# Kernel optimization log

Measured on AMD Instinct MI355X. Metric: run time of the kernel, lower is better.

Reference implementation:

```python
import jax, jax.numpy as jnp
import numpy as np

B, S, H, D = 16, 512, 12, 64          # batch, seq, heads, head_dim
HID = H * D                            # 768
MAX_POS = 512
CHAR_HP = 0.5
WORD_HP = 0.5


def setup_inputs() -> dict:
    key = jax.random.key(0)
    ks = jax.random.split(key, 12)
    s = 0.02
    return {
        "hidden_states": jax.random.normal(ks[0], (B, S, HID), jnp.float32),
        "attention_mask": jnp.zeros((B, 1, 1, S), jnp.float32),
        "character_level_matrix": jax.random.randint(ks[1], (B, S, S), 0, 8),
        "word_level_matrix": jax.random.randint(ks[2], (B, S, S), 0, 8),
        "Wq": jax.random.normal(ks[3], (HID, HID), jnp.float32) * s,
        "bq": jnp.zeros((HID,), jnp.float32),
        "Wk": jax.random.normal(ks[4], (HID, HID), jnp.float32) * s,
        "bk": jnp.zeros((HID,), jnp.float32),
        "Wv": jax.random.normal(ks[5], (HID, HID), jnp.float32) * s,
        "bv": jnp.zeros((HID,), jnp.float32),
        "dist_emb": jax.random.normal(ks[6], (2 * MAX_POS - 1, D), jnp.float32) * s,
        "char_emb": jax.random.normal(ks[7], (8, 1), jnp.float32) * s,
        "word_emb": jax.random.normal(ks[8], (8, 1), jnp.float32) * s,
    }


def reference(hidden_states, attention_mask, character_level_matrix,
              word_level_matrix, Wq, bq, Wk, bk, Wv, bv,
              dist_emb, char_emb, word_emb):
    # level nn-embedding lookup: [B,S,S] int -> [B,S,S] float
    char_bias = char_emb[character_level_matrix][..., 0]
    word_bias = word_emb[word_level_matrix][..., 0]

    def heads(x):  # [B,S,HID] -> [B,H,S,D]
        return x.reshape(B, S, H, D).transpose(0, 2, 1, 3)

    q = heads(hidden_states @ Wq.T + bq)
    k = heads(hidden_states @ Wk.T + bk)
    v = heads(hidden_states @ Wv.T + bv)

    scores = jnp.einsum('bhld,bhrd->bhlr', q, k)
    # level biases broadcast over heads
    scores = scores + CHAR_HP * char_bias[:, None] + WORD_HP * word_bias[:, None]

    # relative_key_query positional scores
    pos = jnp.arange(S)
    distance = pos[:, None] - pos[None, :]
    pe = dist_emb[distance + MAX_POS - 1]  # [S(l), S(r), D]
    scores = scores + jnp.einsum('bhld,lrd->bhlr', q, pe) \
                    + jnp.einsum('bhrd,lrd->bhlr', k, pe)

    scores = scores / jnp.sqrt(jnp.float32(D)) + attention_mask
    probs = jax.nn.softmax(scores, axis=-1)
    ctx = jnp.einsum('bhlr,bhrd->bhld', probs, v)
    return ctx.transpose(0, 2, 1, 3).reshape(B, S, HID)
```

## Files before the change

kernel.cpp:

```cpp
#include <hip/hip_runtime.h>
#include <stdint.h>

#define Bv 16
#define Sv 512
#define Hv 12
#define Dv 64
#define HIDv 768

typedef __attribute__((ext_vector_type(8))) short bf8_t;
typedef __attribute__((ext_vector_type(4))) float f32x4;
typedef __attribute__((ext_vector_type(8))) unsigned short u16x8;
typedef __attribute__((ext_vector_type(4))) unsigned short u16x4;

__device__ __forceinline__ float b2f(unsigned short u){
    union { unsigned int i; float f; } x; x.i = ((unsigned int)u) << 16; return x.f;
}
__device__ __forceinline__ unsigned short f2b(float f){
    union { float f; unsigned int i; } x; x.f = f;
    unsigned int r = x.i + 0x7fff + ((x.i >> 16) & 1);
    return (unsigned short)(r >> 16);
}
__device__ __forceinline__ void gload16(const unsigned short* g, unsigned short* l){
    __builtin_amdgcn_global_load_lds(
        (const __attribute__((address_space(1))) void*)g,
        (__attribute__((address_space(3))) void*)l, 16, 0, 0);
}

#define RS 0.18033688f
#define LOG2E 1.44269504f

__global__ void cvt_bf16(const float* __restrict__ src, unsigned short* __restrict__ dst, int n4){
    int i = blockIdx.x * 256 + threadIdx.x;
    int stride = gridDim.x * 256;
    for (; i < n4; i += stride){
        float4 v = ((const float4*)src)[i];
        u16x4 o = { f2b(v.x), f2b(v.y), f2b(v.z), f2b(v.w) };
        ((u16x4*)dst)[i] = o;
    }
}

__global__ void cvt_w3(const float* __restrict__ a, const float* __restrict__ b,
                       const float* __restrict__ c, unsigned short* __restrict__ dst, int n4each){
    int i = blockIdx.x * 256 + threadIdx.x;
    if (i >= 3*n4each) return;
    int which = i / n4each, j = i - which*n4each;
    const float* src = which == 0 ? a : (which == 1 ? b : c);
    float4 v = ((const float4*)src)[j];
    u16x4 o = { f2b(v.x), f2b(v.y), f2b(v.z), f2b(v.w) };
    ((u16x4*)dst)[i] = o;
}

__global__ __launch_bounds__(256) void prep_bias_t(
    const int* __restrict__ cmat, const int* __restrict__ wmat,
    const float* __restrict__ mask, const float* __restrict__ ce, const float* __restrict__ we,
    unsigned short* __restrict__ lvlt)
{
    __shared__ float tab[64];
    __shared__ float mrow[64];
    const int t = threadIdx.x;
    const int blk = blockIdx.x;
    const int c8 = blk & 7, lt = (blk >> 3) & 7, b = blk >> 6;
    if (t < 64) tab[t] = (0.5f*ce[t>>3] + 0.5f*we[t&7]) * RS;
    if (t >= 64 && t < 128) mrow[t-64] = mask[b*512 + c8*64 + (t-64)] * LOG2E;
    __syncthreads();
    const int w = t >> 6, lane = t & 63, g = lane >> 4, cc = lane & 15;
    const int llb = lt*64 + w*16 + g*4;
    const int rlb = c8*64 + cc;
    unsigned short o[16];
    #pragma unroll
    for (int reg = 0; reg < 4; ++reg){
        const int* cr = cmat + ((size_t)b*512 + llb + reg)*512 + rlb;
        const int* wr = wmat + ((size_t)b*512 + llb + reg)*512 + rlb;
        #pragma unroll
        for (int i = 0; i < 4; ++i){
            int cv = cr[i*16], wv = wr[i*16];
            o[reg*4 + i] = f2b(tab[(cv<<3)|wv] + mrow[i*16 + cc]);
        }
    }
    unsigned short* dst = lvlt + ((size_t)blk*256 + t)*16;
    *(u16x8*)dst       = *(u16x8*)&o[0];
    *(u16x8*)(dst + 8) = *(u16x8*)&o[8];
}

__global__ __launch_bounds__(256,3) void qkv_gemm(
    const unsigned short* __restrict__ Xb,
    const unsigned short* __restrict__ Wb,
    const float* __restrict__ bq, const float* __restrict__ bk, const float* __restrict__ bv,
    unsigned short* __restrict__ qkb,
    unsigned short* __restrict__ vtb)
{
    __shared__ unsigned short Ab[128*40];
    __shared__ unsigned short Bb[128*40];
    const int t = threadIdx.x;
    const int w = t >> 6, lane = t & 63, g = lane >> 4, cc = lane & 15;
    const int wm = w >> 1, wn = w & 1;
    const int m0 = blockIdx.x * 128;
    const int n0 = blockIdx.y * 128;

    const f32x4 fz = {0.f,0.f,0.f,0.f};
    f32x4 acc[4][4];
    #pragma unroll
    for (int i = 0; i < 4; ++i)
        #pragma unroll
        for (int j = 0; j < 4; ++j) acc[i][j] = fz;

    u16x8 pa[2], pb[2];
    #pragma unroll
    for (int r = 0; r < 2; ++r){
        int chunk = t + r*256; int row = chunk >> 2; int ch = chunk & 3;
        pa[r] = *(const u16x8*)(Xb + (size_t)(m0+row)*768 + ch*8);
        pb[r] = *(const u16x8*)(Wb + (size_t)(n0+row)*768 + ch*8);
    }
    for (int k0 = 0; k0 < 768; k0 += 32){
        __syncthreads();
        #pragma unroll
        for (int r = 0; r < 2; ++r){
            int chunk = t + r*256; int row = chunk >> 2; int ch = chunk & 3;
            *(u16x8*)&Ab[row*40 + ch*8] = pa[r];
            *(u16x8*)&Bb[row*40 + ch*8] = pb[r];
        }
        __syncthreads();
        if (k0 + 32 < 768){
            #pragma unroll
            for (int r = 0; r < 2; ++r){
                int chunk = t + r*256; int row = chunk >> 2; int ch = chunk & 3;
                pa[r] = *(const u16x8*)(Xb + (size_t)(m0+row)*768 + (k0+32) + ch*8);
                pb[r] = *(const u16x8*)(Wb + (size_t)(n0+row)*768 + (k0+32) + ch*8);
            }
        }
        bf8_t af[4], bfr[4];
        #pragma unroll
        for (int mf = 0; mf < 4; ++mf)
            af[mf] = *(const bf8_t*)&Ab[(wm*64 + mf*16 + cc)*40 + g*8];
        #pragma unroll
        for (int nf = 0; nf < 4; ++nf)
            bfr[nf] = *(const bf8_t*)&Bb[(wn*64 + nf*16 + cc)*40 + g*8];
        #pragma unroll
        for (int mf = 0; mf < 4; ++mf)
            #pragma unroll
            for (int nf = 0; nf < 4; ++nf)
                acc[mf][nf] = __builtin_amdgcn_mfma_f32_16x16x32_bf16(af[mf], bfr[nf], acc[mf][nf], 0,0,0);
    }

    const int b  = m0 >> 9;
    const int s0 = (m0 & 511) + wm*64;
    const int nbase = n0 + wn*64;
    const int proj = nbase / 768;
    const int nin0 = nbase % 768;
    const float* bias = proj == 0 ? bq : (proj == 1 ? bk : bv);
    #pragma unroll
    for (int nf = 0; nf < 4; ++nf){
        int nin = nin0 + nf*16 + cc;
        int h = nin >> 6, d = nin & 63;
        float bvv = bias[nin];
        #pragma unroll
        for (int mf = 0; mf < 4; ++mf){
            int s = s0 + mf*16 + g*4;
            if (proj < 2){
                unsigned short* base = qkb + (((((size_t)proj*Bv + b)*Hv + h)*Sv + s)*Dv + d);
                #pragma unroll
                for (int r2 = 0; r2 < 4; ++r2)
                    base[(size_t)r2*Dv] = f2b(acc[mf][nf][r2] + bvv);
            } else {
                u16x4 o = { f2b(acc[mf][nf][0]+bvv), f2b(acc[mf][nf][1]+bvv),
                            f2b(acc[mf][nf][2]+bvv), f2b(acc[mf][nf][3]+bvv) };
                *(u16x4*)(vtb + ((((size_t)b*Hv + h)*Dv + d)*Sv + s)) = o;
            }
        }
    }
}

__global__ __launch_bounds__(256,2) void attn(
    const unsigned short* __restrict__ qkb,
    const unsigned short* __restrict__ vtb,
    const unsigned short* __restrict__ deb,
    const unsigned short* __restrict__ lvlt,
    float* __restrict__ out)
{
    __shared__ __align__(16) unsigned short sm[37632];
    unsigned short* ks   = sm;
    unsigned short* vsq  = sm + 4096;
    unsigned short* P    = sm + 12288;
    unsigned short* des  = sm + 16384;
    float*          t1c  = (float*)(sm + 24576);
    unsigned short* t2c  = sm + 33280;

    const int t = threadIdx.x, w = t >> 6, lane = t & 63, g = lane >> 4, cc = lane & 15;
    const int lr8 = lane >> 3, lc8 = lane & 7;

    const int wg = blockIdx.x;
    const int xcd = wg & 7, inner = wg >> 3;
    const int b  = ((inner & 1) << 3) | xcd;
    const int r2 = inner >> 1;
    const int h  = r2 % 12, lt = r2 / 12;
    const int l0 = lt * 64;

    const unsigned short* qp = qkb + ((((size_t)0*Bv + b)*Hv + h)*Sv + l0)*Dv;
    const unsigned short* kp = qkb + ((((size_t)1*Bv + b)*Hv + h)*Sv)*Dv;
    const unsigned short* vp = vtb + (((size_t)b*Hv + h)*Dv)*Sv;
    const unsigned short* lvbase = lvlt + (((size_t)b*8 + lt)*8)*256*16 + (size_t)t*16;

    const f32x4 fz = {0.f,0.f,0.f,0.f};
    const int llb = w*16 + g*4;
    const int R   = 3 - w;
    const int rl2b = R*16 + g*4;

    auto stage_k = [&](int r0){
        #pragma unroll
        for (int j = 0; j < 2; ++j){
            int row = w*16 + j*8 + lr8;
            int ch  = lc8 ^ (row & 7);
            gload16(kp + (size_t)(r0 + row)*64 + ch*8, ks + w*1024 + j*512);
        }
    };
    auto stage_de = [&](int r0){
        const int base = l0 - r0 + 448;
        #pragma unroll
        for (int j = 0; j < 4; ++j){
            int row = w*32 + j*8 + lr8;
            int gr = base + row; if (gr > 1022) gr = 1022;
            int ch  = lc8 ^ (row & 7);
            gload16(deb + (size_t)gr*64 + ch*8, des + w*2048 + j*512);
        }
    };
    auto stage_v = [&](int r0, unsigned short* vdst){
        #pragma unroll
        for (int j = 0; j < 2; ++j){
            int row = w*16 + j*8 + lr8;
            int ch  = lc8 ^ (row & 7);
            gload16(vp + (size_t)row*512 + r0 + ch*8, vdst + w*1024 + j*512);
        }
    };

    bf8_t qf0, qf1;
    {
        int qrow = w*16 + cc;
        qf0 = *(const bf8_t*)(qp + (size_t)qrow*64 + g*8);
        qf1 = *(const bf8_t*)(qp + (size_t)qrow*64 + (g+4)*8);
    }
    stage_k(0); stage_de(0); stage_v(0, vsq);
    __syncthreads();

    float l_run[4] = {0.f,0.f,0.f,0.f};
    f32x4 ctx[4] = {fz,fz,fz,fz};

    for (int c8 = 0; c8 < 8; ++c8){
        const int r0 = c8 * 64;
        unsigned short* vcur = vsq + (c8 & 1) * 4096;
        unsigned short* vnxt = vsq + ((c8 + 1) & 1) * 4096;

        u16x8 lva = *(const u16x8*)(lvbase + (size_t)c8*256*16);
        u16x8 lvb = *(const u16x8*)(lvbase + (size_t)c8*256*16 + 8);

        __builtin_amdgcn_s_setprio(1);
        f32x4 accs[4];
        bf8_t kf0, kf1;
        #pragma unroll
        for (int i = 0; i < 4; ++i){
            int row = i*16 + cc;
            bf8_t b0 = *(const bf8_t*)&ks[row*64 + ((g       ^ (row & 7))*8)];
            bf8_t b1 = *(const bf8_t*)&ks[row*64 + (((g + 4) ^ (row & 7))*8)];
            if (i == R){ kf0 = b0; kf1 = b1; }
            f32x4 a = fz;
            a = __builtin_amdgcn_mfma_f32_16x16x32_bf16(qf0, b0, a, 0,0,0);
            a = __builtin_amdgcn_mfma_f32_16x16x32_bf16(qf1, b1, a, 0,0,0);
            accs[i] = a;
        }
        #pragma unroll
        for (int i = 0; i < 5; ++i){
            int jrow = (w + i)*16 + cc;
            bf8_t d0 = *(const bf8_t*)&des[jrow*64 + ((g       ^ (jrow & 7))*8)];
            bf8_t d1 = *(const bf8_t*)&des[jrow*64 + (((g + 4) ^ (jrow & 7))*8)];
            f32x4 a1 = fz, a2 = fz;
            a1 = __builtin_amdgcn_mfma_f32_16x16x32_bf16(qf0, d0, a1, 0,0,0);
            a1 = __builtin_amdgcn_mfma_f32_16x16x32_bf16(qf1, d1, a1, 0,0,0);
            a2 = __builtin_amdgcn_mfma_f32_16x16x32_bf16(kf0, d0, a2, 0,0,0);
            a2 = __builtin_amdgcn_mfma_f32_16x16x32_bf16(kf1, d1, a2, 0,0,0);
            #pragma unroll
            for (int reg = 0; reg < 4; ++reg){
                int rl1 = 4*g + reg - 16*i - cc + 63;
                if (rl1 >= 0 && rl1 < 64) t1c[rl1*68 + llb + reg] = a1[reg];
                int ll2 = 4*g + reg + 16*i + cc - 15;
                if (ll2 >= 0 && ll2 < 64) t2c[(rl2b + reg)*68 + ll2] = f2b(a2[reg]);
            }
        }
        __builtin_amdgcn_s_setprio(0);
        __syncthreads();

        if (c8 < 7){ stage_k(r0 + 64); stage_de(r0 + 64); stage_v(r0 + 64, vnxt); }

        f32x4 t1v4[4];
        u16x4 t2v4[4];
        #pragma unroll
        for (int i = 0; i < 4; ++i){
            t1v4[i] = *(const f32x4*)&t1c[(16*i + cc)*68 + llb];
            t2v4[i] = *(const u16x4*)&t2c[(16*i + cc)*68 + llb];
        }
        #pragma unroll
        for (int reg = 0; reg < 4; ++reg){
            int ll = llb + reg;
            float ps = 0.f;
            #pragma unroll
            for (int i = 0; i < 4; ++i){
                float lvv = b2f(reg < 2 ? (unsigned short)lva[reg*4 + i]
                                        : (unsigned short)lvb[(reg-2)*4 + i]);
                float sv = (accs[i][reg] + t1v4[i][reg] + b2f((unsigned short)t2v4[i][reg])) * RS + lvv;
                float p = __builtin_amdgcn_exp2f(sv);
                ps += p;
                int rl = i*16 + cc;
                P[ll*64 + (((rl >> 3) ^ (ll & 7)) << 3) + (rl & 7)] = f2b(p);
            }
            ps += __shfl_xor(ps, 1); ps += __shfl_xor(ps, 2);
            ps += __shfl_xor(ps, 4); ps += __shfl_xor(ps, 8);
            l_run[reg] += ps;
        }

        __builtin_amdgcn_s_setprio(1);
        #pragma unroll
        for (int kh = 0; kh < 2; ++kh){
            int prow = w*16 + cc;
            bf8_t pf = *(const bf8_t*)&P[prow*64 + (((g + 4*kh) ^ (prow & 7)) << 3)];
            #pragma unroll
            for (int nf = 0; nf < 4; ++nf){
                int vr = nf*16 + cc;
                bf8_t vf = *(const bf8_t*)&vcur[vr*64 + (((g + 4*kh) ^ (vr & 7))*8)];
                ctx[nf] = __builtin_amdgcn_mfma_f32_16x16x32_bf16(pf, vf, ctx[nf], 0,0,0);
            }
        }
        __builtin_amdgcn_s_setprio(0);

        if (c8 < 7)
            __syncthreads();
    }

    #pragma unroll
    for (int nf = 0; nf < 4; ++nf){
        #pragma unroll
        for (int reg = 0; reg < 4; ++reg){
            int ll = llb + reg;
            out[((size_t)b*Sv + l0 + ll)*HIDv + h*64 + nf*16 + cc] = ctx[nf][reg] / l_run[reg];
        }
    }
}

extern "C" void kernel_launch(void* const* d_in, const int* in_sizes, int n_in,
                              void* d_out, int out_size, void* d_ws, size_t ws_size,
                              hipStream_t stream)
{
    const float* hs   = (const float*)d_in[0];
    const float* mask = (const float*)d_in[1];
    const int*   cmat = (const int*)  d_in[2];
    const int*   wmat = (const int*)  d_in[3];
    const float* Wq   = (const float*)d_in[4];
    const float* bq   = (const float*)d_in[5];
    const float* Wk   = (const float*)d_in[6];
    const float* bk   = (const float*)d_in[7];
    const float* Wv   = (const float*)d_in[8];
    const float* bv   = (const float*)d_in[9];
    const float* de   = (const float*)d_in[10];
    const float* ce   = (const float*)d_in[11];
    const float* we   = (const float*)d_in[12];
    float* out = (float*)d_out;

    unsigned short* Xb   = (unsigned short*)d_ws;
    unsigned short* Wb   = Xb   + 6291456;
    unsigned short* deb  = Wb   + 1769472;
    unsigned short* qkb  = deb  + 65536;
    unsigned short* vtb  = qkb  + 12582912;
    unsigned short* lvlt = vtb  + 6291456;

    cvt_bf16<<<2048, 256, 0, stream>>>(hs, Xb, 1572864);
    cvt_w3<<<1728, 256, 0, stream>>>(Wq, Wk, Wv, Wb, 147456);
    cvt_bf16<<<64,   256, 0, stream>>>(de, deb, 16368);
    prep_bias_t<<<1024, 256, 0, stream>>>(cmat, wmat, mask, ce, we, lvlt);

    qkv_gemm<<<dim3(64, 18), 256, 0, stream>>>(Xb, Wb, bq, bk, bv, qkb, vtb);
    attn<<<1536, 256, 0, stream>>>(qkb, vtb, deb, lvlt, out);
}
```

Measured before the change: 145.3 us.

## Transpose score MFMA outputs, fp32 t2 scratch, register-staged V, vectorized bias prep

Swaps the MFMA operand order for the QK and Q·dist products so each lane holds four consecutive key positions of one query row. This lets P be packed as bf16 pairs and written with one 8-byte store, and reduces the row sum to two shuffles instead of four. The relative-position scratch is rewritten with new index mappings, and t2 is now stored in fp32 instead of bf16. V tiles are no longer double-buffered in LDS through async loads; they are prefetched into registers and written to a single LDS buffer between two extra barriers. The bias-prep kernel now reads int4 and float4 vectors along rows, so memory access is coalesced. These changes trade LDS footprint and extra synchronisation for fewer scattered LDS stores and simpler softmax bookkeeping.

New measurement: 135.7 us. -6.6%, faster.

```diff
diff --git a/kernel.cpp b/kernel.cpp
--- a/kernel.cpp
+++ b/kernel.cpp
@@ -56,26 +56,27 @@
     unsigned short* __restrict__ lvlt)
 {
     __shared__ float tab[64];
-    __shared__ float mrow[64];
     const int t = threadIdx.x;
     const int blk = blockIdx.x;
     const int c8 = blk & 7, lt = (blk >> 3) & 7, b = blk >> 6;
     if (t < 64) tab[t] = (0.5f*ce[t>>3] + 0.5f*we[t&7]) * RS;
-    if (t >= 64 && t < 128) mrow[t-64] = mask[b*512 + c8*64 + (t-64)] * LOG2E;
     __syncthreads();
     const int w = t >> 6, lane = t & 63, g = lane >> 4, cc = lane & 15;
-    const int llb = lt*64 + w*16 + g*4;
-    const int rlb = c8*64 + cc;
+    const int ll = lt*64 + w*16 + cc;
+    const int* crow = cmat + ((size_t)b*512 + ll)*512;
+    const int* wrow = wmat + ((size_t)b*512 + ll)*512;
+    const float* mrow = mask + (size_t)b*512;
     unsigned short o[16];
     #pragma unroll
-    for (int reg = 0; reg < 4; ++reg){
-        const int* cr = cmat + ((size_t)b*512 + llb + reg)*512 + rlb;
-        const int* wr = wmat + ((size_t)b*512 + llb + reg)*512 + rlb;
-        #pragma unroll
-        for (int i = 0; i < 4; ++i){
-            int cv = cr[i*16], wv = wr[i*16];
-            o[reg*4 + i] = f2b(tab[(cv<<3)|wv] + mrow[i*16 + cc]);
-        }
+    for (int i = 0; i < 4; ++i){
+        int rb = c8*64 + i*16 + 4*g;
+        int4 c4 = *(const int4*)(crow + rb);
+        int4 w4 = *(const int4*)(wrow + rb);
+        float4 mv = *(const float4*)(mrow + rb);
+        o[i*4 + 0] = f2b(tab[(c4.x<<3)|w4.x] + mv.x * LOG2E);
+        o[i*4 + 1] = f2b(tab[(c4.y<<3)|w4.y] + mv.y * LOG2E);
+        o[i*4 + 2] = f2b(tab[(c4.z<<3)|w4.z] + mv.z * LOG2E);
+        o[i*4 + 3] = f2b(tab[(c4.w<<3)|w4.w] + mv.w * LOG2E);
     }
     unsigned short* dst = lvlt + ((size_t)blk*256 + t)*16;
     *(u16x8*)dst       = *(u16x8*)&o[0];
@@ -177,13 +178,13 @@
     const unsigned short* __restrict__ lvlt,
     float* __restrict__ out)
 {
-    __shared__ __align__(16) unsigned short sm[37632];
-    unsigned short* ks   = sm;
-    unsigned short* vsq  = sm + 4096;
-    unsigned short* P    = sm + 12288;
-    unsigned short* des  = sm + 16384;
-    float*          t1c  = (float*)(sm + 24576);
-    unsigned short* t2c  = sm + 33280;
+    __shared__ __align__(16) unsigned short sm[37904];
+    unsigned short* ks  = sm;
+    unsigned short* vsq = sm + 4096;
+    unsigned short* des = sm + 8192;
+    float*          t1c = (float*)(sm + 16384);
+    float*          t2c = (float*)(sm + 25360);
+    unsigned int*   Pb  = (unsigned int*)(sm + 33808);
 
     const int t = threadIdx.x, w = t >> 6, lane = t & 63, g = lane >> 4, cc = lane & 15;
     const int lr8 = lane >> 3, lc8 = lane & 7;
@@ -201,9 +202,11 @@
     const unsigned short* lvbase = lvlt + (((size_t)b*8 + lt)*8)*256*16 + (size_t)t*16;
 
     const f32x4 fz = {0.f,0.f,0.f,0.f};
-    const int llb = w*16 + g*4;
     const int R   = 3 - w;
-    const int rl2b = R*16 + g*4;
+    const int llm = w*16 + cc;
+    const int sw  = (cc & 7) << 2;
+    const int d_t1 = cc - 4*g;
+    const int s_t2 = 4*g + cc;
 
     auto stage_k = [&](int r0){
         #pragma unroll
@@ -223,12 +226,12 @@
             gload16(deb + (size_t)gr*64 + ch*8, des + w*2048 + j*512);
         }
     };
-    auto stage_v = [&](int r0, unsigned short* vdst){
+    auto stage_v0 = [&](){
         #pragma unroll
         for (int j = 0; j < 2; ++j){
             int row = w*16 + j*8 + lr8;
             int ch  = lc8 ^ (row & 7);
-            gload16(vp + (size_t)row*512 + r0 + ch*8, vdst + w*1024 + j*512);
+            gload16(vp + (size_t)row*512 + ch*8, vsq + w*1024 + j*512);
         }
     };
 
@@ -238,17 +241,14 @@
         qf0 = *(const bf8_t*)(qp + (size_t)qrow*64 + g*8);
         qf1 = *(const bf8_t*)(qp + (size_t)qrow*64 + (g+4)*8);
     }
-    stage_k(0); stage_de(0); stage_v(0, vsq);
+    stage_k(0); stage_de(0); stage_v0();
     __syncthreads();
 
-    float l_run[4] = {0.f,0.f,0.f,0.f};
+    float l_run = 0.f;
     f32x4 ctx[4] = {fz,fz,fz,fz};
 
     for (int c8 = 0; c8 < 8; ++c8){
         const int r0 = c8 * 64;
-        unsigned short* vcur = vsq + (c8 & 1) * 4096;
-        unsigned short* vnxt = vsq + ((c8 + 1) & 1) * 4096;
-
         u16x8 lva = *(const u16x8*)(lvbase + (size_t)c8*256*16);
         u16x8 lvb = *(const u16x8*)(lvbase + (size_t)c8*256*16 + 8);
 
@@ -262,8 +262,8 @@
             bf8_t b1 = *(const bf8_t*)&ks[row*64 + (((g + 4) ^ (row & 7))*8)];
             if (i == R){ kf0 = b0; kf1 = b1; }
             f32x4 a = fz;
-            a = __builtin_amdgcn_mfma_f32_16x16x32_bf16(qf0, b0, a, 0,0,0);
-            a = __builtin_amdgcn_mfma_f32_16x16x32_bf16(qf1, b1, a, 0,0,0);
+            a = __builtin_amdgcn_mfma_f32_16x16x32_bf16(b0, qf0, a, 0,0,0);
+            a = __builtin_amdgcn_mfma_f32_16x16x32_bf16(b1, qf1, a, 0,0,0);
             accs[i] = a;
         }
         #pragma unroll
@@ -272,73 +272,96 @@
             bf8_t d0 = *(const bf8_t*)&des[jrow*64 + ((g       ^ (jrow & 7))*8)];
             bf8_t d1 = *(const bf8_t*)&des[jrow*64 + (((g + 4) ^ (jrow & 7))*8)];
             f32x4 a1 = fz, a2 = fz;
-            a1 = __builtin_amdgcn_mfma_f32_16x16x32_bf16(qf0, d0, a1, 0,0,0);
-            a1 = __builtin_amdgcn_mfma_f32_16x16x32_bf16(qf1, d1, a1, 0,0,0);
+            a1 = __builtin_amdgcn_mfma_f32_16x16x32_bf16(d0, qf0, a1, 0,0,0);
+            a1 = __builtin_amdgcn_mfma_f32_16x16x32_bf16(d1, qf1, a1, 0,0,0);
             a2 = __builtin_amdgcn_mfma_f32_16x16x32_bf16(kf0, d0, a2, 0,0,0);
             a2 = __builtin_amdgcn_mfma_f32_16x16x32_bf16(kf1, d1, a2, 0,0,0);
-            #pragma unroll
-            for (int reg = 0; reg < 4; ++reg){
-                int rl1 = 4*g + reg - 16*i - cc + 63;
-                if (rl1 >= 0 && rl1 < 64) t1c[rl1*68 + llb + reg] = a1[reg];
-                int ll2 = 4*g + reg + 16*i + cc - 15;
-                if (ll2 >= 0 && ll2 < 64) t2c[(rl2b + reg)*68 + ll2] = f2b(a2[reg]);
+
+            {
+                float* tb = t1c + (cc - 16*i - 4*g + 61)*68 + llm;
+                bool mA = (i != 0 || d_t1 <= 3) && (i != 4 || d_t1 >= 3);
+                bool mB = (i != 0 || d_t1 <= 1) && (i != 4 || d_t1 >= 1);
+                if (mA){ tb[0]   = a1[3]; tb[68]  = a1[2]; }
+                if (mB){ tb[136] = a1[1]; tb[204] = a1[0]; }
+            }
+            {
+                float* tb = t2c + (R*16 + 4*g)*66 + (16*i + 4*g + cc - 14);
+                bool mA = (i != 0 || s_t2 >= 14) && (i != 4 || s_t2 <= 14);
+                bool mB = (i != 0 || s_t2 >= 12) && (i != 4 || s_t2 <= 12);
+                if (mA){ tb[0]   = a2[0]; tb[67]  = a2[1]; }
+                if (mB){ tb[134] = a2[2]; tb[201] = a2[3]; }
             }
         }
         __builtin_amdgcn_s_setprio(0);
         __syncthreads();
 
-        if (c8 < 7){ stage_k(r0 + 64); stage_de(r0 + 64); stage_v(r0 + 64, vnxt); }
-
-        f32x4 t1v4[4];
-        u16x4 t2v4[4];
+        u16x8 pv0, pv1;
+        if (c8 < 7){
+            stage_k(r0 + 64); stage_de(r0 + 64);
+            int row0 = w*16 + lr8,  ch0 = lc8 ^ (row0 & 7);
+            int row1 = row0 + 8,    ch1 = lc8 ^ (row1 & 7);
+            pv0 = *(const u16x8*)(vp + (size_t)row0*512 + (r0+64) + ch0*8);
+            pv1 = *(const u16x8*)(vp + (size_t)row1*512 + (r0+64) + ch1*8);
+        }
+
+        float ps = 0.f;
         #pragma unroll
         for (int i = 0; i < 4; ++i){
-            t1v4[i] = *(const f32x4*)&t1c[(16*i + cc)*68 + llb];
-            t2v4[i] = *(const u16x4*)&t2c[(16*i + cc)*68 + llb];
-        }
-        #pragma unroll
-        for (int reg = 0; reg < 4; ++reg){
-            int ll = llb + reg;
-            float ps = 0.f;
-            #pragma unroll
-            for (int i = 0; i < 4; ++i){
-                float lvv = b2f(reg < 2 ? (unsigned short)lva[reg*4 + i]
-                                        : (unsigned short)lvb[(reg-2)*4 + i]);
-                float sv = (accs[i][reg] + t1v4[i][reg] + b2f((unsigned short)t2v4[i][reg])) * RS + lvv;
-                float p = __builtin_amdgcn_exp2f(sv);
-                ps += p;
-                int rl = i*16 + cc;
-                P[ll*64 + (((rl >> 3) ^ (ll & 7)) << 3) + (rl & 7)] = f2b(p);
-            }
-            ps += __shfl_xor(ps, 1); ps += __shfl_xor(ps, 2);
-            ps += __shfl_xor(ps, 4); ps += __shfl_xor(ps, 8);
-            l_run[reg] += ps;
-        }
+            const float* g1 = t1c + (i*16 + 4*g + 1)*68 + llm;
+            const float* g2 = t2c + (i*16 + 4*g)*66 + llm + 1;
+            float t10 = g1[0], t11 = g1[68], t12 = g1[136], t13 = g1[204];
+            float t20 = g2[0], t21 = g2[66], t22 = g2[132], t23 = g2[198];
+            float lv0 = b2f(i < 2 ? (unsigned short)lva[i*4+0] : (unsigned short)lvb[(i-2)*4+0]);
+            float lv1 = b2f(i < 2 ? (unsigned short)lva[i*4+1] : (unsigned short)lvb[(i-2)*4+1]);
+            float lv2 = b2f(i < 2 ? (unsigned short)lva[i*4+2] : (unsigned short)lvb[(i-2)*4+2]);
+            float lv3 = b2f(i < 2 ? (unsigned short)lva[i*4+3] : (unsigned short)lvb[(i-2)*4+3]);
+            float p0 = __builtin_amdgcn_exp2f((accs[i][0] + t10 + t20) * RS + lv0);
+            float p1 = __builtin_amdgcn_exp2f((accs[i][1] + t11 + t21) * RS + lv1);
+            float p2 = __builtin_amdgcn_exp2f((accs[i][2] + t12 + t22) * RS + lv2);
+            float p3 = __builtin_amdgcn_exp2f((accs[i][3] + t13 + t23) * RS + lv3);
+            ps += (p0 + p1) + (p2 + p3);
+            unsigned int prs0 = (unsigned)f2b(p0) | ((unsigned)f2b(p1) << 16);
+            unsigned int prs1 = (unsigned)f2b(p2) | ((unsigned)f2b(p3) << 16);
+            uint2 pr = { prs0, prs1 };
+            *(uint2*)&Pb[llm*32 + ((i*8 + 2*g) ^ sw)] = pr;
+        }
+        ps += __shfl_xor(ps, 16);
+        ps += __shfl_xor(ps, 32);
+        l_run += ps;
+        __builtin_amdgcn_wave_barrier();
 
         __builtin_amdgcn_s_setprio(1);
         #pragma unroll
         for (int kh = 0; kh < 2; ++kh){
-            int prow = w*16 + cc;
-            bf8_t pf = *(const bf8_t*)&P[prow*64 + (((g + 4*kh) ^ (prow & 7)) << 3)];
+            bf8_t pf = *(const bf8_t*)&Pb[llm*32 + ((16*kh + 4*g) ^ sw)];
             #pragma unroll
             for (int nf = 0; nf < 4; ++nf){
                 int vr = nf*16 + cc;
-                bf8_t vf = *(const bf8_t*)&vcur[vr*64 + (((g + 4*kh) ^ (vr & 7))*8)];
+                bf8_t vf = *(const bf8_t*)&vsq[vr*64 + (((g + 4*kh) ^ (vr & 7))*8)];
                 ctx[nf] = __builtin_amdgcn_mfma_f32_16x16x32_bf16(pf, vf, ctx[nf], 0,0,0);
             }
         }
         __builtin_amdgcn_s_setprio(0);
 
-        if (c8 < 7)
+        if (c8 < 7){
             __syncthreads();
-    }
+            *(u16x8*)&vsq[w*1024 +       lane*8] = pv0;
+            *(u16x8*)&vsq[w*1024 + 512 + lane*8] = pv1;
+            __syncthreads();
+        }
+    }
+
+    float linv[4];
+    #pragma unroll
+    for (int reg = 0; reg < 4; ++reg)
+        linv[reg] = 1.0f / __shfl(l_run, 4*g + reg);
 
     #pragma unroll
     for (int nf = 0; nf < 4; ++nf){
         #pragma unroll
         for (int reg = 0; reg < 4; ++reg){
-            int ll = llb + reg;
-            out[((size_t)b*Sv + l0 + ll)*HIDv + h*64 + nf*16 + cc] = ctx[nf][reg] / l_run[reg];
+            int ll = w*16 + 4*g + reg;
+            out[((size_t)b*Sv + l0 + ll)*HIDv + h*64 + nf*16 + cc] = ctx[nf][reg] * linv[reg];
         }
     }
 }
```
